# Optimization experiments

Measured on AMD Instinct MI355X. Metric: run time of the kernel, lower is better.

## Reference

```python
import jax, jax.numpy as jnp
import numpy as np

EPS = 1e-5        # torch LayerNorm default eps
INNER = 4
AFFECT_W = 0.3
BATCH = 65536
DIM = 128


def _ln(x, g, b):
    m = jnp.mean(x, axis=-1, keepdims=True)
    v = jnp.var(x, axis=-1, keepdims=True)
    return (x - m) * jax.lax.rsqrt(v + EPS) * g + b


def _gelu(x):
    return jax.nn.gelu(x, approximate=False)  # torch nn.GELU default (erf)


def setup_inputs() -> dict:
    key = jax.random.key(0)
    ks = jax.random.split(key, 18)
    B, d = BATCH, DIM

    def W(k, i, o):
        return jax.random.normal(k, (i, o), jnp.float32) / np.float32(np.sqrt(i))

    return {
        "x": jax.random.normal(ks[0], (B, d), jnp.float32),
        "y_init": jax.random.normal(ks[1], (B, d), jnp.float32),
        "affect_vec": jax.random.normal(ks[2], (B, 3), jnp.float32),
        "ln_latent_g": jnp.ones((3 * d,), jnp.float32), "ln_latent_b": jnp.zeros((3 * d,), jnp.float32),
        "ln_answer_g": jnp.ones((2 * d,), jnp.float32), "ln_answer_b": jnp.zeros((2 * d,), jnp.float32),
        "ln_z_g": jnp.ones((d,), jnp.float32), "ln_z_b": jnp.zeros((d,), jnp.float32),
        "lat_w1": W(ks[3], 3 * d, 2 * d), "lat_b1": jnp.zeros((2 * d,), jnp.float32),
        "lat_w2": W(ks[4], 2 * d, d), "lat_b2": jnp.zeros((d,), jnp.float32),
        "ans_w1": W(ks[5], 2 * d, 2 * d), "ans_b1": jnp.zeros((2 * d,), jnp.float32),
        "ans_w2": W(ks[6], 2 * d, d), "ans_b2": jnp.zeros((d,), jnp.float32),
        "aff_w": W(ks[7], 3, d), "aff_b": jnp.zeros((d,), jnp.float32),
        "gate_w": W(ks[8], 2 * d, 1), "gate_b": jnp.zeros((1,), jnp.float32),
        "q_w": W(ks[9], d, d), "q_b": jnp.zeros((d,), jnp.float32),
        "k_w": W(ks[10], d, d), "k_b": jnp.zeros((d,), jnp.float32),
        "v_w": W(ks[11], d, d), "v_b": jnp.zeros((d,), jnp.float32),
        "o_w": W(ks[12], d, d), "o_b": jnp.zeros((d,), jnp.float32),
        "pad_w1": W(ks[13], d, d // 2), "pad_b1": jnp.zeros((d // 2,), jnp.float32),
        "pad_w2": W(ks[14], d // 2, 3), "pad_b2": jnp.zeros((3,), jnp.float32),
        "K": 5,
    }


def _forward(x, y_init, affect_vec, ln_latent_g, ln_latent_b, ln_answer_g, ln_answer_b,
             ln_z_g, ln_z_b, lat_w1, lat_b1, lat_w2, lat_b2, ans_w1, ans_b1, ans_w2, ans_b2,
             aff_w, aff_b, gate_w, gate_b, q_w, q_b, k_w, k_b, v_w, v_b, o_w, o_b,
             pad_w1, pad_b1, pad_w2, pad_b2, K):
    d = x.shape[-1]
    scale = jnp.float32(d) ** -0.5
    y = y_init
    z = jnp.zeros_like(y)
    confs = []     # scalar gate means (detached, like .item() in torch)
    history = []   # list of [B, 1, d] z snapshots
    memory = []    # SoulKernel memory buffer: list of [d] rinse_state[0] snapshots
    for _ in range(K):
        for _ in range(INNER):
            li = _ln(jnp.concatenate([x, y, z], axis=-1), ln_latent_g, ln_latent_b)
            z_delta = _gelu(li @ lat_w1 + lat_b1) @ lat_w2 + lat_b2
            z = _ln(z + 0.3 * z_delta, ln_z_g, ln_z_b)
        affect_latent = jnp.tanh(affect_vec @ aff_w + aff_b)          # [B, d]
        gate = jax.nn.sigmoid(jnp.concatenate([z, affect_latent], axis=-1) @ gate_w + gate_b)  # [B, 1]
        z = z + AFFECT_W * gate * affect_latent
        confs.append(jax.lax.stop_gradient(jnp.mean(gate)))
        history.append(z[:, None, :])
        if len(history) > 1:
            seq = jnp.concatenate(history, axis=1)  # [B, t, d]
            Q = seq @ q_w + q_b
            Kt = seq @ k_w + k_b
            V = seq @ v_w + v_b
            attn = jax.nn.softmax(jnp.einsum('bsd,btd->bst', Q, Kt) * scale, axis=-1)
            attn_out = jnp.einsum('bst,btd->bsd', attn, V) @ o_w + o_b
            z = _ln(z + attn_out[:, -1, :], ln_z_g, ln_z_b)
        rinse = jnp.tanh(z + y)
        # SoulKernel (hope is computed but unused in the original)
        faith = jnp.sqrt(sum(confs) / len(confs))
        z = z + faith * 0.05 * z
        future = jnp.mean(jnp.stack(memory[-3:]), axis=0) if memory else jnp.zeros((d,), x.dtype)  # [d]
        bond = jnp.tanh(jax.lax.stop_gradient(jnp.mean(x * z)) + jax.lax.stop_gradient(jnp.mean(y * rinse)))
        z = z + 0.2 * bond * (future - z)
        rinse = jnp.tanh(rinse + future * 0.3)
        memory.append(jax.lax.stop_gradient(rinse[0]))
        ai = _ln(jnp.concatenate([y, z], axis=-1), ln_answer_g, ln_answer_b)
        y = y + 0.4 * (_gelu(ai @ ans_w1 + ans_b1) @ ans_w2 + ans_b2)
    pad = jnp.tanh(_gelu(z @ pad_w1 + pad_b1) @ pad_w2 + pad_b2)
    return y, jnp.stack(confs), pad


def reference(x, y_init, affect_vec, ln_latent_g, ln_latent_b, ln_answer_g, ln_answer_b,
              ln_z_g, ln_z_b, lat_w1, lat_b1, lat_w2, lat_b2, ans_w1, ans_b1, ans_w2, ans_b2,
              aff_w, aff_b, gate_w, gate_b, q_w, q_b, k_w, k_b, v_w, v_b, o_w, o_b,
              pad_w1, pad_b1, pad_w2, pad_b2, K):
    return _forward(x, y_init, affect_vec, ln_latent_g, ln_latent_b, ln_answer_g, ln_answer_b,
                    ln_z_g, ln_z_b, lat_w1, lat_b1, lat_w2, lat_b2, ans_w1, ans_b1, ans_w2, ans_b2,
                    aff_w, aff_b, gate_w, gate_b, q_w, q_b, k_w, k_b, v_w, v_b, o_w, o_b,
                    pad_w1, pad_b1, pad_w2, pad_b2, K)
```

## Files before the change

### kernel.cpp

```cpp
#include <hip/hip_runtime.h>
#include <math.h>


#define BATCH 65536
#define D 128
#define NSTEP 5
#define ROWS 32
#define NTHR 256
#define NBLK (BATCH / ROWS)
#define LN_EPS 1e-5f
#define ATT_SCALE 0.08838834764831845f
#define LDA 132
#define LDB 260

#define WS_Z    ((size_t)0)
#define WS_ZH   ((size_t)BATCH * D)
#define WS_PART (WS_ZH + (size_t)NSTEP * BATCH * D)
#define WS_SCAL (WS_PART + (size_t)NBLK * 4)
#define SC_FS   0
#define SC_B02  1
#define SC_CSUM 2
#define SC_FUT  16
#define SC_MEM  256
#define SC_R10  960

struct Args {
  const float *x, *y_init, *affect;
  const float *g_lat, *b_lat, *g_ans, *b_ans, *g_z, *b_z;
  const float *lw1, *lb1, *lw2, *lb2;
  const float *aw1, *ab1, *aw2, *ab2;
  const float *affw, *affb, *gw, *gb;
  const float *qw, *qb, *kw, *kb, *vw, *vb, *ow, *ob;
  const float *pw1, *pb1, *pw2, *pb2;
  float *Y, *conf, *pad;
  float *Z, *ZH, *PART, *SCAL;
};

__device__ __forceinline__ float4 ld4(const float* p) { return *(const float4*)p; }
__device__ __forceinline__ void st4(float* p, float4 v) { *(float4*)p = v; }
__device__ __forceinline__ float geluf(float v) { return 0.5f*v*(1.0f + erff(v*0.70710678118654752f)); }
__device__ __forceinline__ float dot4(float4 a, float4 b){ return a.x*b.x + a.y*b.y + a.z*b.z + a.w*b.w; }
__device__ __forceinline__ void accSQ(float4 v, float& S, float& Q) {
  S += v.x+v.y+v.z+v.w;
  Q += v.x*v.x + v.y*v.y + v.z*v.z + v.w*v.w;
}

template<int KDIM, int NPT>
__device__ __forceinline__ void mm_block(const float* __restrict__ W, int N,
                                         const float* As, int lda,
                                         int rg, int cg, float (&acc)[4][NPT])
{
  const float* a0 = As + (rg*4+0)*lda;
  const float* a1 = As + (rg*4+1)*lda;
  const float* a2 = As + (rg*4+2)*lda;
  const float* a3 = As + (rg*4+3)*lda;
  const float* wp = W + cg*NPT;
  #pragma unroll 4
  for (int k = 0; k < KDIM; ++k) {
    float w[NPT];
    if constexpr (NPT == 8) {
      float4 w0 = ld4(wp + (size_t)k*N);
      float4 w1 = ld4(wp + (size_t)k*N + 4);
      w[0]=w0.x; w[1]=w0.y; w[2]=w0.z; w[3]=w0.w;
      w[4]=w1.x; w[5]=w1.y; w[6]=w1.z; w[7]=w1.w;
    } else if constexpr (NPT == 4) {
      float4 w0 = ld4(wp + (size_t)k*N);
      w[0]=w0.x; w[1]=w0.y; w[2]=w0.z; w[3]=w0.w;
    } else {
      float2 w0 = *(const float2*)(wp + (size_t)k*N);
      w[0]=w0.x; w[1]=w0.y;
    }
    float av0=a0[k], av1=a1[k], av2=a2[k], av3=a3[k];
    #pragma unroll
    for (int c = 0; c < NPT; ++c) {
      acc[0][c] += av0*w[c];
      acc[1][c] += av1*w[c];
      acc[2][c] += av2*w[c];
      acc[3][c] += av3*w[c];
    }
  }
}

__device__ __forceinline__ void z_ln_update(const Args& A, int row0, int rg, int cg,
                                            const float (&add)[4][4])
{
  float4 g4 = ld4(A.g_z + cg*4);
  float4 b4 = ld4(A.b_z + cg*4);
  #pragma unroll
  for (int rr = 0; rr < 4; ++rr) {
    size_t off = (size_t)(row0 + rg*4 + rr)*D + cg*4;
    float4 z = ld4(A.Z + off);
    float v0 = z.x + add[rr][0];
    float v1 = z.y + add[rr][1];
    float v2 = z.z + add[rr][2];
    float v3 = z.w + add[rr][3];
    float S = v0+v1+v2+v3;
    float Q = v0*v0+v1*v1+v2*v2+v3*v3;
    S += __shfl_xor(S,1);  Q += __shfl_xor(Q,1);
    S += __shfl_xor(S,2);  Q += __shfl_xor(Q,2);
    S += __shfl_xor(S,4);  Q += __shfl_xor(Q,4);
    S += __shfl_xor(S,8);  Q += __shfl_xor(Q,8);
    S += __shfl_xor(S,16); Q += __shfl_xor(Q,16);
    float m  = S*(1.f/128.f);
    float rs = rsqrtf(Q*(1.f/128.f) - m*m + LN_EPS);
    float4 o;
    o.x = (v0-m)*rs*g4.x + b4.x;
    o.y = (v1-m)*rs*g4.y + b4.y;
    o.z = (v2-m)*rs*g4.z + b4.z;
    o.w = (v3-m)*rs*g4.w + b4.w;
    st4(A.Z + off, o);
  }
}

__device__ __forceinline__ void stage_raw(float* sA, const float* src, int row0, int t)
{
  for (int e4 = t; e4 < ROWS*32; e4 += NTHR) {
    int r = e4 >> 5, c4 = e4 & 31;
    st4(sA + r*LDA + c4*4, ld4(src + (size_t)(row0+r)*D + c4*4));
  }
}

__device__ __forceinline__ void epilogue_phase(const Args& A, float* sB, float* sM, float* sR,
                                               int row0, int t, int rg, int cg, int r8, int sub)
{
  const float fs  = A.SCAL[SC_FS];
  const float b02 = A.SCAL[SC_B02];
  const float a   = fs*(1.0f - b02);
  for (int e4 = t; e4 < ROWS*32; e4 += NTHR) {
    int r = e4 >> 5, c4 = e4 & 31;
    size_t off = (size_t)(row0 + r)*D + c4*4;
    float4 z = ld4(A.Z + off);
    float4 f = ld4(A.SCAL + SC_FUT + c4*4);
    z.x = z.x*a + b02*f.x;
    z.y = z.y*a + b02*f.y;
    z.z = z.z*a + b02*f.z;
    z.w = z.w*a + b02*f.w;
    st4(A.Z + off, z);
  }
  __syncthreads();
  {
    const float* yr = A.Y + (size_t)(row0 + r8)*D;
    const float* zr = A.Z + (size_t)(row0 + r8)*D;
    float S = 0.f, Q = 0.f;
    #pragma unroll
    for (int j = 0; j < 4; ++j) {
      int c = (sub + 8*j)*4;
      accSQ(ld4(yr + c), S, Q);
      accSQ(ld4(zr + c), S, Q);
    }
    S += __shfl_xor(S,1); Q += __shfl_xor(Q,1);
    S += __shfl_xor(S,2); Q += __shfl_xor(Q,2);
    S += __shfl_xor(S,4); Q += __shfl_xor(Q,4);
    if (sub == 0) {
      float m = S*(1.f/256.f);
      sM[r8] = m;
      sR[r8] = rsqrtf(Q*(1.f/256.f) - m*m + LN_EPS);
    }
  }
  __syncthreads();
  for (int e4 = t; e4 < ROWS*64; e4 += NTHR) {
    int r = e4 >> 6, c4 = e4 & 63;
    int k = c4*4;
    float m = sM[r], rs = sR[r];
    float4 v = (k < D) ? ld4(A.Y + (size_t)(row0+r)*D + k)
                       : ld4(A.Z + (size_t)(row0+r)*D + (k - D));
    float4 g = ld4(A.g_ans + k);
    float4 b = ld4(A.b_ans + k);
    float4 o;
    o.x = (v.x-m)*rs*g.x + b.x;
    o.y = (v.y-m)*rs*g.y + b.y;
    o.z = (v.z-m)*rs*g.z + b.z;
    o.w = (v.w-m)*rs*g.w + b.w;
    st4(sB + r*LDB + k, o);
  }
  __syncthreads();
  float acc[4][8] = {};
  mm_block<256,8>(A.aw1, 256, sB, LDB, rg, cg, acc);
  float4 b1a = ld4(A.ab1 + cg*8);
  float4 b1b = ld4(A.ab1 + cg*8 + 4);
  float h[4][8];
  #pragma unroll
  for (int rr = 0; rr < 4; ++rr) {
    h[rr][0]=geluf(acc[rr][0]+b1a.x); h[rr][1]=geluf(acc[rr][1]+b1a.y);
    h[rr][2]=geluf(acc[rr][2]+b1a.z); h[rr][3]=geluf(acc[rr][3]+b1a.w);
    h[rr][4]=geluf(acc[rr][4]+b1b.x); h[rr][5]=geluf(acc[rr][5]+b1b.y);
    h[rr][6]=geluf(acc[rr][6]+b1b.z); h[rr][7]=geluf(acc[rr][7]+b1b.w);
  }
  __syncthreads();
  #pragma unroll
  for (int rr = 0; rr < 4; ++rr) {
    float4 h0; h0.x=h[rr][0]; h0.y=h[rr][1]; h0.z=h[rr][2]; h0.w=h[rr][3];
    float4 h1; h1.x=h[rr][4]; h1.y=h[rr][5]; h1.z=h[rr][6]; h1.w=h[rr][7];
    st4(sB + (rg*4+rr)*LDB + cg*8,     h0);
    st4(sB + (rg*4+rr)*LDB + cg*8 + 4, h1);
  }
  __syncthreads();
  float acc2[4][4] = {};
  mm_block<256,4>(A.aw2, 128, sB, LDB, rg, cg, acc2);
  float4 b2 = ld4(A.ab2 + cg*4);
  #pragma unroll
  for (int rr = 0; rr < 4; ++rr) {
    size_t off = (size_t)(row0 + rg*4 + rr)*D + cg*4;
    float4 y = ld4(A.Y + off);
    y.x += 0.4f*(acc2[rr][0] + b2.x);
    y.y += 0.4f*(acc2[rr][1] + b2.y);
    y.z += 0.4f*(acc2[rr][2] + b2.z);
    y.w += 0.4f*(acc2[rr][3] + b2.w);
    st4(A.Y + off, y);
  }
  __syncthreads();
}

__global__ void prepK(Args A)
{
  size_t i  = (size_t)blockIdx.x*blockDim.x + threadIdx.x;
  size_t n4 = (size_t)BATCH*D/4;
  float4 zero; zero.x=0.f; zero.y=0.f; zero.z=0.f; zero.w=0.f;
  for (; i < n4; i += (size_t)gridDim.x*blockDim.x) {
    ((float4*)A.Z)[i] = zero;
    ((float4*)A.Y)[i] = ((const float4*)A.y_init)[i];
  }
}

template<int STEP>
__global__ __launch_bounds__(NTHR, 2) void stepK(Args A)
{
  __shared__ __align__(16) float sA[ROWS*LDA];
  __shared__ __align__(16) float sB[ROWS*LDB];
  __shared__ float sM[ROWS], sR[ROWS], sG[ROWS];
  __shared__ float sS[ROWS][8];
  __shared__ float sRed[4][2];

  const int t = threadIdx.x;
  const int row0 = blockIdx.x * ROWS;
  const int rg = t >> 5, cg = t & 31;
  const int r8 = t >> 3, sub = t & 7;

  if (STEP > 0)
    epilogue_phase(A, sB, sM, sR, row0, t, rg, cg, r8, sub);

  #pragma unroll 1
  for (int it = 0; it < 4; ++it) {
    {
      const float* xr = A.x + (size_t)(row0 + r8)*D;
      const float* yr = A.Y + (size_t)(row0 + r8)*D;
      const float* zr = A.Z + (size_t)(row0 + r8)*D;
      float S = 0.f, Q = 0.f;
      #pragma unroll
      for (int j = 0; j < 4; ++j) {
        int c = (sub + 8*j)*4;
        accSQ(ld4(xr + c), S, Q);
        accSQ(ld4(yr + c), S, Q);
        accSQ(ld4(zr + c), S, Q);
      }
      S += __shfl_xor(S,1); Q += __shfl_xor(Q,1);
      S += __shfl_xor(S,2); Q += __shfl_xor(Q,2);
      S += __shfl_xor(S,4); Q += __shfl_xor(Q,4);
      if (sub == 0) {
        float m = S*(1.f/384.f);
        sM[r8] = m;
        sR[r8] = rsqrtf(Q*(1.f/384.f) - m*m + LN_EPS);
      }
    }
    __syncthreads();
    float acc[4][8] = {};
    #pragma unroll 1
    for (int seg = 0; seg < 3; ++seg) {
      const float* src = (seg == 0) ? A.x : (seg == 1 ? (const float*)A.Y : (const float*)A.Z);
      for (int e4 = t; e4 < ROWS*32; e4 += NTHR) {
        int r = e4 >> 5, c4 = e4 & 31;
        float4 v = ld4(src + (size_t)(row0+r)*D + c4*4);
        float m = sM[r], rs = sR[r];
        int k = seg*D + c4*4;
        float4 g = ld4(A.g_lat + k);
        float4 b = ld4(A.b_lat + k);
        float4 o;
        o.x = (v.x-m)*rs*g.x + b.x;
        o.y = (v.y-m)*rs*g.y + b.y;
        o.z = (v.z-m)*rs*g.z + b.z;
        o.w = (v.w-m)*rs*g.w + b.w;
        st4(sA + r*LDA + c4*4, o);
      }
      __syncthreads();
      mm_block<128,8>(A.lw1 + (size_t)seg*D*256, 256, sA, LDA, rg, cg, acc);
      __syncthreads();
    }
    float4 l1a = ld4(A.lb1 + cg*8);
    float4 l1b = ld4(A.lb1 + cg*8 + 4);
    #pragma unroll
    for (int rr = 0; rr < 4; ++rr) {
      float4 h0, h1;
      h0.x = geluf(acc[rr][0]+l1a.x); h0.y = geluf(acc[rr][1]+l1a.y);
      h0.z = geluf(acc[rr][2]+l1a.z); h0.w = geluf(acc[rr][3]+l1a.w);
      h1.x = geluf(acc[rr][4]+l1b.x); h1.y = geluf(acc[rr][5]+l1b.y);
      h1.z = geluf(acc[rr][6]+l1b.z); h1.w = geluf(acc[rr][7]+l1b.w);
      st4(sB + (rg*4+rr)*LDB + cg*8,     h0);
      st4(sB + (rg*4+rr)*LDB + cg*8 + 4, h1);
    }
    __syncthreads();
    float acc2[4][4] = {};
    mm_block<256,4>(A.lw2, 128, sB, LDB, rg, cg, acc2);
    float4 l2 = ld4(A.lb2 + cg*4);
    float add[4][4];
    #pragma unroll
    for (int rr = 0; rr < 4; ++rr) {
      add[rr][0] = 0.3f*(acc2[rr][0]+l2.x);
      add[rr][1] = 0.3f*(acc2[rr][1]+l2.y);
      add[rr][2] = 0.3f*(acc2[rr][2]+l2.z);
      add[rr][3] = 0.3f*(acc2[rr][3]+l2.w);
    }
    z_ln_update(A, row0, rg, cg, add);
    __syncthreads();
  }

  {
    size_t row = (size_t)row0 + r8;
    const float* zr = A.Z + row*D;
    float af0 = A.affect[row*3+0];
    float af1 = A.affect[row*3+1];
    float af2 = A.affect[row*3+2];
    float dg = 0.f;
    #pragma unroll
    for (int j = 0; j < 4; ++j) {
      int c = (sub + 8*j)*4;
      float4 zv = ld4(zr + c);
      float4 g1 = ld4(A.gw + c);
      float4 g2 = ld4(A.gw + D + c);
      float4 w0 = ld4(A.affw + c);
      float4 w1 = ld4(A.affw + D + c);
      float4 w2 = ld4(A.affw + 2*D + c);
      float4 ab = ld4(A.affb + c);
      float4 al;
      al.x = tanhf(af0*w0.x + af1*w1.x + af2*w2.x + ab.x);
      al.y = tanhf(af0*w0.y + af1*w1.y + af2*w2.y + ab.y);
      al.z = tanhf(af0*w0.z + af1*w1.z + af2*w2.z + ab.z);
      al.w = tanhf(af0*w0.w + af1*w1.w + af2*w2.w + ab.w);
      st4(sA + r8*LDA + c, al);
      dg += dot4(zv, g1) + dot4(al, g2);
    }
    dg += __shfl_xor(dg,1);
    dg += __shfl_xor(dg,2);
    dg += __shfl_xor(dg,4);
    if (sub == 0) sG[r8] = 1.f/(1.f + expf(-(dg + A.gb[0])));
  }
  __syncthreads();
  {
    float* zhw = A.ZH + (size_t)STEP*BATCH*D;
    for (int e4 = t; e4 < ROWS*32; e4 += NTHR) {
      int r = e4 >> 5, c4 = e4 & 31;
      size_t off = (size_t)(row0+r)*D + c4*4;
      float4 z  = ld4(A.Z + off);
      float4 al = ld4(sA + r*LDA + c4*4);
      float g = 0.3f * sG[r];
      z.x += g*al.x; z.y += g*al.y; z.z += g*al.z; z.w += g*al.w;
      st4(A.Z + off, z);
      st4(zhw + off, z);
    }
  }
  __syncthreads();

  if (STEP > 0) {
    stage_raw(sA, A.Z, row0, t);
    __syncthreads();
    float qacc[4][4] = {};
    mm_block<128,4>(A.qw, 128, sA, LDA, rg, cg, qacc);
    float4 qb4 = ld4(A.qb + cg*4);
    #pragma unroll
    for (int rr = 0; rr < 4; ++rr) {
      float4 q;
      q.x=qacc[rr][0]+qb4.x; q.y=qacc[rr][1]+qb4.y;
      q.z=qacc[rr][2]+qb4.z; q.w=qacc[rr][3]+qb4.w;
      st4(sB + (rg*4+rr)*LDB + cg*4, q);
    }
    __syncthreads();
    #pragma unroll 1
    for (int j = 0; j <= STEP; ++j) {
      stage_raw(sA, A.ZH + (size_t)j*BATCH*D, row0, t);
      __syncthreads();
      float kacc[4][4] = {};
      mm_block<128,4>(A.kw, 128, sA, LDA, rg, cg, kacc);
      float4 kb4 = ld4(A.kb + cg*4);
      #pragma unroll
      for (int rr = 0; rr < 4; ++rr) {
        const float* qrow = sB + (rg*4+rr)*LDB + cg*4;
        float s = qrow[0]*(kacc[rr][0]+kb4.x) + qrow[1]*(kacc[rr][1]+kb4.y)
                + qrow[2]*(kacc[rr][2]+kb4.z) + qrow[3]*(kacc[rr][3]+kb4.w);
        s += __shfl_xor(s,1); s += __shfl_xor(s,2); s += __shfl_xor(s,4);
        s += __shfl_xor(s,8); s += __shfl_xor(s,16);
        if (cg == 0) sS[rg*4+rr][j] = s;
      }
      __syncthreads();
    }
    if (t < ROWS) {
      float mx = -3.0e38f;
      for (int j = 0; j <= STEP; ++j) { float v = sS[t][j]*ATT_SCALE; sS[t][j] = v; mx = fmaxf(mx, v); }
      float sum = 0.f;
      for (int j = 0; j <= STEP; ++j) { float p = expf(sS[t][j]-mx); sS[t][j] = p; sum += p; }
      float inv = 1.f/sum;
      for (int j = 0; j <= STEP; ++j) sS[t][j] *= inv;
    }
    __syncthreads();
    float ao[4][4] = {};
    #pragma unroll 1
    for (int j = 0; j <= STEP; ++j) {
      stage_raw(sA, A.ZH + (size_t)j*BATCH*D, row0, t);
      __syncthreads();
      float vacc[4][4] = {};
      mm_block<128,4>(A.vw, 128, sA, LDA, rg, cg, vacc);
      float4 vb4 = ld4(A.vb + cg*4);
      #pragma unroll
      for (int rr = 0; rr < 4; ++rr) {
        float p = sS[rg*4+rr][j];
        ao[rr][0] += p*(vacc[rr][0]+vb4.x);
        ao[rr][1] += p*(vacc[rr][1]+vb4.y);
        ao[rr][2] += p*(vacc[rr][2]+vb4.z);
        ao[rr][3] += p*(vacc[rr][3]+vb4.w);
      }
      __syncthreads();
    }
    #pragma unroll
    for (int rr = 0; rr < 4; ++rr) {
      float4 v; v.x=ao[rr][0]; v.y=ao[rr][1]; v.z=ao[rr][2]; v.w=ao[rr][3];
      st4(sA + (rg*4+rr)*LDA + cg*4, v);
    }
    __syncthreads();
    float oacc[4][4] = {};
    mm_block<128,4>(A.ow, 128, sA, LDA, rg, cg, oacc);
    float4 ob4 = ld4(A.ob + cg*4);
    float add[4][4];
    #pragma unroll
    for (int rr = 0; rr < 4; ++rr) {
      add[rr][0] = oacc[rr][0]+ob4.x;
      add[rr][1] = oacc[rr][1]+ob4.y;
      add[rr][2] = oacc[rr][2]+ob4.z;
      add[rr][3] = oacc[rr][3]+ob4.w;
    }
    z_ln_update(A, row0, rg, cg, add);
    __syncthreads();
  }

  {
    float sxz = 0.f, syr = 0.f;
    for (int e4 = t; e4 < ROWS*32; e4 += NTHR) {
      int r = e4 >> 5, c4 = e4 & 31;
      size_t off = (size_t)(row0+r)*D + c4*4;
      float4 xv = ld4(A.x + off);
      float4 zv = ld4(A.Z + off);
      float4 yv = ld4(A.Y + off);
      float4 rn;
      rn.x = tanhf(zv.x + yv.x);
      rn.y = tanhf(zv.y + yv.y);
      rn.z = tanhf(zv.z + yv.z);
      rn.w = tanhf(zv.w + yv.w);
      sxz += dot4(xv, zv);
      syr += dot4(yv, rn);
      if (blockIdx.x == 0 && r == 0)
        st4(A.SCAL + SC_R10 + c4*4, rn);
    }
    #pragma unroll
    for (int m2 = 1; m2 < 64; m2 <<= 1) { sxz += __shfl_xor(sxz,m2); syr += __shfl_xor(syr,m2); }
    if ((t & 63) == 0) { sRed[t>>6][0] = sxz; sRed[t>>6][1] = syr; }
    __syncthreads();
    if (t == 0) {
      float X = 0.f, Yv = 0.f, G = 0.f;
      #pragma unroll
      for (int w2 = 0; w2 < 4; ++w2) { X += sRed[w2][0]; Yv += sRed[w2][1]; }
      #pragma unroll
      for (int r = 0; r < ROWS; ++r) G += sG[r];
      float* p = A.PART + (size_t)blockIdx.x*4;
      p[0] = G; p[1] = X; p[2] = Yv;
    }
  }
}

template<int STEP>
__global__ void redK(Args A)
{
  __shared__ float sRed[4][3];
  const int t = threadIdx.x;
  float sg = 0.f, sxz = 0.f, syr = 0.f;
  for (int b = t; b < NBLK; b += 256) {
    const float* p = A.PART + (size_t)b*4;
    sg += p[0]; sxz += p[1]; syr += p[2];
  }
  #pragma unroll
  for (int m = 1; m < 64; m <<= 1) {
    sg  += __shfl_xor(sg,m);
    sxz += __shfl_xor(sxz,m);
    syr += __shfl_xor(syr,m);
  }
  if ((t & 63) == 0) { int w = t>>6; sRed[w][0]=sg; sRed[w][1]=sxz; sRed[w][2]=syr; }
  __syncthreads();
  if (t == 0) {
    float G=0.f, X=0.f, Yv=0.f;
    #pragma unroll
    for (int w = 0; w < 4; ++w) { G += sRed[w][0]; X += sRed[w][1]; Yv += sRed[w][2]; }
    float conf = G * (1.f/(float)BATCH);
    float csum = conf + (STEP == 0 ? 0.f : A.SCAL[SC_CSUM]);
    A.SCAL[SC_CSUM] = csum;
    A.conf[STEP] = conf;
    float faith = sqrtf(csum / (float)(STEP+1));
    float fs = 1.f + 0.05f*faith;
    float bond = tanhf((fs*X + Yv) * (1.f/((float)BATCH*(float)D)));
    A.SCAL[SC_FS]  = fs;
    A.SCAL[SC_B02] = 0.2f*bond;
  }
  if (t < D) {
    float fut = 0.f;
    if (STEP > 0) {
      int lo = (STEP-3 < 0) ? 0 : STEP-3;
      float s = 0.f;
      for (int j = lo; j < STEP; ++j) s += A.SCAL[SC_MEM + j*D + t];
      fut = s / (float)(STEP - lo);
    }
    A.SCAL[SC_FUT + t] = fut;
    A.SCAL[SC_MEM + STEP*D + t] = tanhf(A.SCAL[SC_R10 + t] + 0.3f*fut);
  }
}

__global__ __launch_bounds__(NTHR, 2) void finalK(Args A)
{
  __shared__ __align__(16) float sA[ROWS*LDA];
  __shared__ __align__(16) float sB[ROWS*LDB];
  __shared__ float sM[ROWS], sR[ROWS];
  const int t = threadIdx.x;
  const int row0 = blockIdx.x * ROWS;
  const int rg = t >> 5, cg = t & 31;
  const int r8 = t >> 3, sub = t & 7;

  epilogue_phase(A, sB, sM, sR, row0, t, rg, cg, r8, sub);

  stage_raw(sA, A.Z, row0, t);
  __syncthreads();
  float acc[4][2] = {};
  mm_block<128,2>(A.pw1, 64, sA, LDA, rg, cg, acc);
  float2 pb = *(const float2*)(A.pb1 + cg*2);
  #pragma unroll
  for (int rr = 0; rr < 4; ++rr) {
    sB[(rg*4+rr)*LDB + cg*2 + 0] = geluf(acc[rr][0] + pb.x);
    sB[(rg*4+rr)*LDB + cg*2 + 1] = geluf(acc[rr][1] + pb.y);
  }
  __syncthreads();
  {
    float o0=0.f, o1=0.f, o2=0.f;
    #pragma unroll
    for (int jj = 0; jj < 8; ++jj) {
      int j = sub*8 + jj;
      float p = sB[r8*LDB + j];
      o0 += p*A.pw2[j*3+0];
      o1 += p*A.pw2[j*3+1];
      o2 += p*A.pw2[j*3+2];
    }
    o0 += __shfl_xor(o0,1); o0 += __shfl_xor(o0,2); o0 += __shfl_xor(o0,4);
    o1 += __shfl_xor(o1,1); o1 += __shfl_xor(o1,2); o1 += __shfl_xor(o1,4);
    o2 += __shfl_xor(o2,1); o2 += __shfl_xor(o2,2); o2 += __shfl_xor(o2,4);
    if (sub == 0) {
      size_t ro = (size_t)(row0 + r8)*3;
      A.pad[ro+0] = tanhf(o0 + A.pb2[0]);
      A.pad[ro+1] = tanhf(o1 + A.pb2[1]);
      A.pad[ro+2] = tanhf(o2 + A.pb2[2]);
    }
  }
}

extern "C" void kernel_launch(void* const* d_in, const int* in_sizes, int n_in,
                              void* d_out, int out_size, void* d_ws, size_t ws_size,
                              hipStream_t stream)
{
  (void)in_sizes; (void)n_in; (void)out_size; (void)ws_size;
  Args a;
  a.x      = (const float*)d_in[0];
  a.y_init = (const float*)d_in[1];
  a.affect = (const float*)d_in[2];
  a.g_lat  = (const float*)d_in[3];
  a.b_lat  = (const float*)d_in[4];
  a.g_ans  = (const float*)d_in[5];
  a.b_ans  = (const float*)d_in[6];
  a.g_z    = (const float*)d_in[7];
  a.b_z    = (const float*)d_in[8];
  a.lw1    = (const float*)d_in[9];
  a.lb1    = (const float*)d_in[10];
  a.lw2    = (const float*)d_in[11];
  a.lb2    = (const float*)d_in[12];
  a.aw1    = (const float*)d_in[13];
  a.ab1    = (const float*)d_in[14];
  a.aw2    = (const float*)d_in[15];
  a.ab2    = (const float*)d_in[16];
  a.affw   = (const float*)d_in[17];
  a.affb   = (const float*)d_in[18];
  a.gw     = (const float*)d_in[19];
  a.gb     = (const float*)d_in[20];
  a.qw     = (const float*)d_in[21];
  a.qb     = (const float*)d_in[22];
  a.kw     = (const float*)d_in[23];
  a.kb     = (const float*)d_in[24];
  a.vw     = (const float*)d_in[25];
  a.vb     = (const float*)d_in[26];
  a.ow     = (const float*)d_in[27];
  a.ob     = (const float*)d_in[28];
  a.pw1    = (const float*)d_in[29];
  a.pb1    = (const float*)d_in[30];
  a.pw2    = (const float*)d_in[31];
  a.pb2    = (const float*)d_in[32];
  float* out = (float*)d_out;
  a.Y    = out;
  a.conf = out + (size_t)BATCH*D;
  a.pad  = a.conf + NSTEP;
  float* ws = (float*)d_ws;
  a.Z    = ws + WS_Z;
  a.ZH   = ws + WS_ZH;
  a.PART = ws + WS_PART;
  a.SCAL = ws + WS_SCAL;

  prepK<<<dim3(2048), dim3(256), 0, stream>>>(a);
  stepK<0><<<dim3(NBLK), dim3(NTHR), 0, stream>>>(a);
  redK<0><<<dim3(1), dim3(256), 0, stream>>>(a);
  stepK<1><<<dim3(NBLK), dim3(NTHR), 0, stream>>>(a);
  redK<1><<<dim3(1), dim3(256), 0, stream>>>(a);
  stepK<2><<<dim3(NBLK), dim3(NTHR), 0, stream>>>(a);
  redK<2><<<dim3(1), dim3(256), 0, stream>>>(a);
  stepK<3><<<dim3(NBLK), dim3(NTHR), 0, stream>>>(a);
  redK<3><<<dim3(1), dim3(256), 0, stream>>>(a);
  stepK<4><<<dim3(NBLK), dim3(NTHR), 0, stream>>>(a);
  redK<4><<<dim3(1), dim3(256), 0, stream>>>(a);
  finalK<<<dim3(NBLK), dim3(NTHR), 0, stream>>>(a);
}
```

Measured before the change: 8.326 ms.

## Merge shared buffers into one tile and raise occupancy to four blocks per CU

Collapses the two shared-memory tiles (sA, sB) into one unified buffer sU and raises launch bounds from 2 to 4 blocks per multiprocessor, which cuts LDS per block roughly in half. Query projections are kept in registers rather than shared memory, and barriers inside the attention loops move so the single buffer can be reused safely. Fixed-count staging loops are also unrolled. The tighter launch bound can force register spilling and adds barriers where the buffers used to be separate.

After: 10.24 ms. +23.0%, slower.

```diff
diff --git a/kernel.cpp b/kernel.cpp
--- a/kernel.cpp
+++ b/kernel.cpp
@@ -4,19 +4,20 @@
 
 #define BATCH 65536
 #define D 128
+#define BD ((size_t)BATCH * D)
 #define NSTEP 5
 #define ROWS 32
 #define NTHR 256
 #define NBLK (BATCH / ROWS)
 #define LN_EPS 1e-5f
 #define ATT_SCALE 0.08838834764831845f
-#define LDA 132
-#define LDB 260
+#define LDU 260
 
 #define WS_Z    ((size_t)0)
-#define WS_ZH   ((size_t)BATCH * D)
-#define WS_PART (WS_ZH + (size_t)NSTEP * BATCH * D)
-#define WS_SCAL (WS_PART + (size_t)NBLK * 4)
+#define WS_ZH   (BD)
+#define WS_PART (WS_ZH + 5*BD)
+#define WS_SCAL (WS_PART + (size_t)NBLK*4)
+
 #define SC_FS   0
 #define SC_B02  1
 #define SC_CSUM 2
@@ -112,21 +113,25 @@
   }
 }
 
-__device__ __forceinline__ void stage_raw(float* sA, const float* src, int row0, int t)
-{
-  for (int e4 = t; e4 < ROWS*32; e4 += NTHR) {
+__device__ __forceinline__ void stage_raw(float* sU, const float* src, int row0, int t)
+{
+  #pragma unroll
+  for (int p = 0; p < 4; ++p) {
+    int e4 = t + p*NTHR;
     int r = e4 >> 5, c4 = e4 & 31;
-    st4(sA + r*LDA + c4*4, ld4(src + (size_t)(row0+r)*D + c4*4));
-  }
-}
-
-__device__ __forceinline__ void epilogue_phase(const Args& A, float* sB, float* sM, float* sR,
+    st4(sU + r*LDU + c4*4, ld4(src + (size_t)(row0+r)*D + c4*4));
+  }
+}
+
+__device__ __forceinline__ void epilogue_phase(const Args& A, float* sU, float* sM, float* sR,
                                                int row0, int t, int rg, int cg, int r8, int sub)
 {
   const float fs  = A.SCAL[SC_FS];
   const float b02 = A.SCAL[SC_B02];
   const float a   = fs*(1.0f - b02);
-  for (int e4 = t; e4 < ROWS*32; e4 += NTHR) {
+  #pragma unroll
+  for (int p = 0; p < 4; ++p) {
+    int e4 = t + p*NTHR;
     int r = e4 >> 5, c4 = e4 & 31;
     size_t off = (size_t)(row0 + r)*D + c4*4;
     float4 z = ld4(A.Z + off);
@@ -171,11 +176,11 @@
     o.y = (v.y-m)*rs*g.y + b.y;
     o.z = (v.z-m)*rs*g.z + b.z;
     o.w = (v.w-m)*rs*g.w + b.w;
-    st4(sB + r*LDB + k, o);
+    st4(sU + r*LDU + k, o);
   }
   __syncthreads();
   float acc[4][8] = {};
-  mm_block<256,8>(A.aw1, 256, sB, LDB, rg, cg, acc);
+  mm_block<256,8>(A.aw1, 256, sU, LDU, rg, cg, acc);
   float4 b1a = ld4(A.ab1 + cg*8);
   float4 b1b = ld4(A.ab1 + cg*8 + 4);
   float h[4][8];
@@ -191,12 +196,12 @@
   for (int rr = 0; rr < 4; ++rr) {
     float4 h0; h0.x=h[rr][0]; h0.y=h[rr][1]; h0.z=h[rr][2]; h0.w=h[rr][3];
     float4 h1; h1.x=h[rr][4]; h1.y=h[rr][5]; h1.z=h[rr][6]; h1.w=h[rr][7];
-    st4(sB + (rg*4+rr)*LDB + cg*8,     h0);
-    st4(sB + (rg*4+rr)*LDB + cg*8 + 4, h1);
+    st4(sU + (rg*4+rr)*LDU + cg*8,     h0);
+    st4(sU + (rg*4+rr)*LDU + cg*8 + 4, h1);
   }
   __syncthreads();
   float acc2[4][4] = {};
-  mm_block<256,4>(A.aw2, 128, sB, LDB, rg, cg, acc2);
+  mm_block<256,4>(A.aw2, 128, sU, LDU, rg, cg, acc2);
   float4 b2 = ld4(A.ab2 + cg*4);
   #pragma unroll
   for (int rr = 0; rr < 4; ++rr) {
@@ -214,7 +219,7 @@
 __global__ void prepK(Args A)
 {
   size_t i  = (size_t)blockIdx.x*blockDim.x + threadIdx.x;
-  size_t n4 = (size_t)BATCH*D/4;
+  size_t n4 = BD/4;
   float4 zero; zero.x=0.f; zero.y=0.f; zero.z=0.f; zero.w=0.f;
   for (; i < n4; i += (size_t)gridDim.x*blockDim.x) {
     ((float4*)A.Z)[i] = zero;
@@ -223,10 +228,9 @@
 }
 
 template<int STEP>
-__global__ __launch_bounds__(NTHR, 2) void stepK(Args A)
-{
-  __shared__ __align__(16) float sA[ROWS*LDA];
-  __shared__ __align__(16) float sB[ROWS*LDB];
+__global__ __launch_bounds__(NTHR, 4) void stepK(Args A)
+{
+  __shared__ __align__(16) float sU[ROWS*LDU];
   __shared__ float sM[ROWS], sR[ROWS], sG[ROWS];
   __shared__ float sS[ROWS][8];
   __shared__ float sRed[4][2];
@@ -237,7 +241,7 @@
   const int r8 = t >> 3, sub = t & 7;
 
   if (STEP > 0)
-    epilogue_phase(A, sB, sM, sR, row0, t, rg, cg, r8, sub);
+    epilogue_phase(A, sU, sM, sR, row0, t, rg, cg, r8, sub);
 
   #pragma unroll 1
   for (int it = 0; it < 4; ++it) {
@@ -267,7 +271,9 @@
     #pragma unroll 1
     for (int seg = 0; seg < 3; ++seg) {
       const float* src = (seg == 0) ? A.x : (seg == 1 ? (const float*)A.Y : (const float*)A.Z);
-      for (int e4 = t; e4 < ROWS*32; e4 += NTHR) {
+      #pragma unroll
+      for (int p = 0; p < 4; ++p) {
+        int e4 = t + p*NTHR;
         int r = e4 >> 5, c4 = e4 & 31;
         float4 v = ld4(src + (size_t)(row0+r)*D + c4*4);
         float m = sM[r], rs = sR[r];
@@ -279,10 +285,10 @@
         o.y = (v.y-m)*rs*g.y + b.y;
         o.z = (v.z-m)*rs*g.z + b.z;
         o.w = (v.w-m)*rs*g.w + b.w;
-        st4(sA + r*LDA + c4*4, o);
+        st4(sU + r*LDU + c4*4, o);
       }
       __syncthreads();
-      mm_block<128,8>(A.lw1 + (size_t)seg*D*256, 256, sA, LDA, rg, cg, acc);
+      mm_block<128,8>(A.lw1 + (size_t)seg*D*256, 256, sU, LDU, rg, cg, acc);
       __syncthreads();
     }
     float4 l1a = ld4(A.lb1 + cg*8);
@@ -294,12 +300,12 @@
       h0.z = geluf(acc[rr][2]+l1a.z); h0.w = geluf(acc[rr][3]+l1a.w);
       h1.x = geluf(acc[rr][4]+l1b.x); h1.y = geluf(acc[rr][5]+l1b.y);
       h1.z = geluf(acc[rr][6]+l1b.z); h1.w = geluf(acc[rr][7]+l1b.w);
-      st4(sB + (rg*4+rr)*LDB + cg*8,     h0);
-      st4(sB + (rg*4+rr)*LDB + cg*8 + 4, h1);
+      st4(sU + (rg*4+rr)*LDU + cg*8,     h0);
+      st4(sU + (rg*4+rr)*LDU + cg*8 + 4, h1);
     }
     __syncthreads();
     float acc2[4][4] = {};
-    mm_block<256,4>(A.lw2, 128, sB, LDB, rg, cg, acc2);
+    mm_block<256,4>(A.lw2, 128, sU, LDU, rg, cg, acc2);
     float4 l2 = ld4(A.lb2 + cg*4);
     float add[4][4];
     #pragma unroll
@@ -335,7 +341,7 @@
       al.y = tanhf(af0*w0.y + af1*w1.y + af2*w2.y + ab.y);
       al.z = tanhf(af0*w0.z + af1*w1.z + af2*w2.z + ab.z);
       al.w = tanhf(af0*w0.w + af1*w1.w + af2*w2.w + ab.w);
-      st4(sA + r8*LDA + c, al);
+      st4(sU + r8*LDU + c, al);
       dg += dot4(zv, g1) + dot4(al, g2);
     }
     dg += __shfl_xor(dg,1);
@@ -345,12 +351,14 @@
   }
   __syncthreads();
   {
-    float* zhw = A.ZH + (size_t)STEP*BATCH*D;
-    for (int e4 = t; e4 < ROWS*32; e4 += NTHR) {
+    float* zhw = A.ZH + (size_t)STEP*BD;
+    #pragma unroll
+    for (int p = 0; p < 4; ++p) {
+      int e4 = t + p*NTHR;
       int r = e4 >> 5, c4 = e4 & 31;
       size_t off = (size_t)(row0+r)*D + c4*4;
       float4 z  = ld4(A.Z + off);
-      float4 al = ld4(sA + r*LDA + c4*4);
+      float4 al = ld4(sU + r*LDU + c4*4);
       float g = 0.3f * sG[r];
       z.x += g*al.x; z.y += g*al.y; z.z += g*al.z; z.w += g*al.w;
       st4(A.Z + off, z);
@@ -360,37 +368,37 @@
   __syncthreads();
 
   if (STEP > 0) {
-    stage_raw(sA, A.Z, row0, t);
-    __syncthreads();
-    float qacc[4][4] = {};
-    mm_block<128,4>(A.qw, 128, sA, LDA, rg, cg, qacc);
-    float4 qb4 = ld4(A.qb + cg*4);
-    #pragma unroll
-    for (int rr = 0; rr < 4; ++rr) {
-      float4 q;
-      q.x=qacc[rr][0]+qb4.x; q.y=qacc[rr][1]+qb4.y;
-      q.z=qacc[rr][2]+qb4.z; q.w=qacc[rr][3]+qb4.w;
-      st4(sB + (rg*4+rr)*LDB + cg*4, q);
-    }
-    __syncthreads();
+    stage_raw(sU, A.Z, row0, t);
+    __syncthreads();
+    float q[4][4];
+    {
+      float qacc[4][4] = {};
+      mm_block<128,4>(A.qw, 128, sU, LDU, rg, cg, qacc);
+      float4 qb4 = ld4(A.qb + cg*4);
+      #pragma unroll
+      for (int rr = 0; rr < 4; ++rr) {
+        q[rr][0]=qacc[rr][0]+qb4.x; q[rr][1]=qacc[rr][1]+qb4.y;
+        q[rr][2]=qacc[rr][2]+qb4.z; q[rr][3]=qacc[rr][3]+qb4.w;
+      }
+    }
     #pragma unroll 1
     for (int j = 0; j <= STEP; ++j) {
-      stage_raw(sA, A.ZH + (size_t)j*BATCH*D, row0, t);
+      __syncthreads();
+      stage_raw(sU, A.ZH + (size_t)j*BD, row0, t);
       __syncthreads();
       float kacc[4][4] = {};
-      mm_block<128,4>(A.kw, 128, sA, LDA, rg, cg, kacc);
+      mm_block<128,4>(A.kw, 128, sU, LDU, rg, cg, kacc);
       float4 kb4 = ld4(A.kb + cg*4);
       #pragma unroll
       for (int rr = 0; rr < 4; ++rr) {
-        const float* qrow = sB + (rg*4+rr)*LDB + cg*4;
-        float s = qrow[0]*(kacc[rr][0]+kb4.x) + qrow[1]*(kacc[rr][1]+kb4.y)
-                + qrow[2]*(kacc[rr][2]+kb4.z) + qrow[3]*(kacc[rr][3]+kb4.w);
+        float s = q[rr][0]*(kacc[rr][0]+kb4.x) + q[rr][1]*(kacc[rr][1]+kb4.y)
+                + q[rr][2]*(kacc[rr][2]+kb4.z) + q[rr][3]*(kacc[rr][3]+kb4.w);
         s += __shfl_xor(s,1); s += __shfl_xor(s,2); s += __shfl_xor(s,4);
         s += __shfl_xor(s,8); s += __shfl_xor(s,16);
         if (cg == 0) sS[rg*4+rr][j] = s;
       }
-      __syncthreads();
-    }
+    }
+    __syncthreads();
     if (t < ROWS) {
       float mx = -3.0e38f;
       for (int j = 0; j <= STEP; ++j) { float v = sS[t][j]*ATT_SCALE; sS[t][j] = v; mx = fmaxf(mx, v); }
@@ -403,10 +411,11 @@
     float ao[4][4] = {};
     #pragma unroll 1
     for (int j = 0; j <= STEP; ++j) {
-      stage_raw(sA, A.ZH + (size_t)j*BATCH*D, row0, t);
+      __syncthreads();
+      stage_raw(sU, A.ZH + (size_t)j*BD, row0, t);
       __syncthreads();
       float vacc[4][4] = {};
-      mm_block<128,4>(A.vw, 128, sA, LDA, rg, cg, vacc);
+      mm_block<128,4>(A.vw, 128, sU, LDU, rg, cg, vacc);
       float4 vb4 = ld4(A.vb + cg*4);
       #pragma unroll
       for (int rr = 0; rr < 4; ++rr) {
@@ -416,16 +425,16 @@
         ao[rr][2] += p*(vacc[rr][2]+vb4.z);
         ao[rr][3] += p*(vacc[rr][3]+vb4.w);
       }
-      __syncthreads();
-    }
+    }
+    __syncthreads();
     #pragma unroll
     for (int rr = 0; rr < 4; ++rr) {
       float4 v; v.x=ao[rr][0]; v.y=ao[rr][1]; v.z=ao[rr][2]; v.w=ao[rr][3];
-      st4(sA + (rg*4+rr)*LDA + cg*4, v);
+      st4(sU + (rg*4+rr)*LDU + cg*4, v);
     }
     __syncthreads();
     float oacc[4][4] = {};
-    mm_block<128,4>(A.ow, 128, sA, LDA, rg, cg, oacc);
+    mm_block<128,4>(A.ow, 128, sU, LDU, rg, cg, oacc);
     float4 ob4 = ld4(A.ob + cg*4);
     float add[4][4];
     #pragma unroll
@@ -441,7 +450,9 @@
 
   {
     float sxz = 0.f, syr = 0.f;
-    for (int e4 = t; e4 < ROWS*32; e4 += NTHR) {
+    #pragma unroll
+    for (int p = 0; p < 4; ++p) {
+      int e4 = t + p*NTHR;
       int r = e4 >> 5, c4 = e4 & 31;
       size_t off = (size_t)(row0+r)*D + c4*4;
       float4 xv = ld4(A.x + off);
@@ -518,27 +529,27 @@
   }
 }
 
-__global__ __launch_bounds__(NTHR, 2) void finalK(Args A)
-{
-  __shared__ __align__(16) float sA[ROWS*LDA];
-  __shared__ __align__(16) float sB[ROWS*LDB];
+__global__ __launch_bounds__(NTHR, 4) void finalK(Args A)
+{
+  __shared__ __align__(16) float sU[ROWS*LDU];
   __shared__ float sM[ROWS], sR[ROWS];
   const int t = threadIdx.x;
   const int row0 = blockIdx.x * ROWS;
   const int rg = t >> 5, cg = t & 31;
   const int r8 = t >> 3, sub = t & 7;
 
-  epilogue_phase(A, sB, sM, sR, row0, t, rg, cg, r8, sub);
-
-  stage_raw(sA, A.Z, row0, t);
+  epilogue_phase(A, sU, sM, sR, row0, t, rg, cg, r8, sub);
+
+  stage_raw(sU, A.Z, row0, t);
   __syncthreads();
   float acc[4][2] = {};
-  mm_block<128,2>(A.pw1, 64, sA, LDA, rg, cg, acc);
+  mm_block<128,2>(A.pw1, 64, sU, LDU, rg, cg, acc);
   float2 pb = *(const float2*)(A.pb1 + cg*2);
+  __syncthreads();
   #pragma unroll
   for (int rr = 0; rr < 4; ++rr) {
-    sB[(rg*4+rr)*LDB + cg*2 + 0] = geluf(acc[rr][0] + pb.x);
-    sB[(rg*4+rr)*LDB + cg*2 + 1] = geluf(acc[rr][1] + pb.y);
+    sU[(rg*4+rr)*LDU + 128 + cg*2 + 0] = geluf(acc[rr][0] + pb.x);
+    sU[(rg*4+rr)*LDU + 128 + cg*2 + 1] = geluf(acc[rr][1] + pb.y);
   }
   __syncthreads();
   {
@@ -546,7 +557,7 @@
     #pragma unroll
     for (int jj = 0; jj < 8; ++jj) {
       int j = sub*8 + jj;
-      float p = sB[r8*LDB + j];
+      float p = sU[r8*LDU + 128 + j];
       o0 += p*A.pw2[j*3+0];
       o1 += p*A.pw2[j*3+1];
       o2 += p*A.pw2[j*3+2];
@@ -604,7 +615,7 @@
   a.pb2    = (const float*)d_in[32];
   float* out = (float*)d_out;
   a.Y    = out;
-  a.conf = out + (size_t)BATCH*D;
+  a.conf = out + BD;
   a.pad  = a.conf + NSTEP;
   float* ws = (float*)d_ws;
   a.Z    = ws + WS_Z;
```

## Cache per-step K/V projections in workspace instead of recomputing history

Applied to the files above, without the earlier changes.

When the workspace is large enough, each step computes K and V projections of the new z once and stores them, so later steps read cached K/V rather than re-projecting every past z through k_w and v_w. This removes a quadratic number of small matmuls per block at the cost of extra workspace memory and global reads. The change also stages all three LayerNorm segments at once to cut barriers in the latent matmul, unrolls the staging loops, and raises the launch-bounds occupancy hint to 3 blocks per CU, which may force register spills. A fallback path keeps the recompute behaviour when the workspace is too small.

Result: slower. 11.36 ms (+36.4%).

```diff
diff --git a/kernel.cpp b/kernel.cpp
--- a/kernel.cpp
+++ b/kernel.cpp
@@ -4,6 +4,7 @@
 
 #define BATCH 65536
 #define D 128
+#define BD ((size_t)BATCH * D)
 #define NSTEP 5
 #define ROWS 32
 #define NTHR 256
@@ -14,9 +15,12 @@
 #define LDB 260
 
 #define WS_Z    ((size_t)0)
-#define WS_ZH   ((size_t)BATCH * D)
-#define WS_PART (WS_ZH + (size_t)NSTEP * BATCH * D)
-#define WS_SCAL (WS_PART + (size_t)NBLK * 4)
+#define WS_H1   (BD)
+#define WS_PART (WS_H1 + 5*BD)
+#define WS_SCAL (WS_PART + (size_t)NBLK*4)
+#define WS_H2   (WS_SCAL + 2048)
+#define WS_KV_END (WS_H2 + 5*BD)
+
 #define SC_FS   0
 #define SC_B02  1
 #define SC_CSUM 2
@@ -33,7 +37,8 @@
   const float *qw, *qb, *kw, *kb, *vw, *vb, *ow, *ob;
   const float *pw1, *pb1, *pw2, *pb2;
   float *Y, *conf, *pad;
-  float *Z, *ZH, *PART, *SCAL;
+  float *Z, *H1, *H2, *PART, *SCAL;
+  int useKV;
 };
 
 __device__ __forceinline__ float4 ld4(const float* p) { return *(const float4*)p; }
@@ -114,9 +119,51 @@
 
 __device__ __forceinline__ void stage_raw(float* sA, const float* src, int row0, int t)
 {
-  for (int e4 = t; e4 < ROWS*32; e4 += NTHR) {
+  #pragma unroll
+  for (int p = 0; p < 4; ++p) {
+    int e4 = t + p*NTHR;
     int r = e4 >> 5, c4 = e4 & 31;
     st4(sA + r*LDA + c4*4, ld4(src + (size_t)(row0+r)*D + c4*4));
+  }
+}
+
+__device__ __forceinline__ void stage_cat(const Args& A, float* sA, float* sB,
+                                          int row0, int t, const float* sM, const float* sR)
+{
+  #pragma unroll
+  for (int p = 0; p < 4; ++p) {
+    int e4 = t + p*NTHR;
+    int r = e4 >> 5, c4 = e4 & 31;
+    float m = sM[r], rs = sR[r];
+    size_t roff = (size_t)(row0+r)*D + c4*4;
+    int k0 = c4*4;
+    {
+      float4 v = ld4(A.x + roff);
+      float4 g = ld4(A.g_lat + k0);
+      float4 b = ld4(A.b_lat + k0);
+      float4 o;
+      o.x=(v.x-m)*rs*g.x+b.x; o.y=(v.y-m)*rs*g.y+b.y;
+      o.z=(v.z-m)*rs*g.z+b.z; o.w=(v.w-m)*rs*g.w+b.w;
+      st4(sA + r*LDA + k0, o);
+    }
+    {
+      float4 v = ld4(A.Y + roff);
+      float4 g = ld4(A.g_lat + D + k0);
+      float4 b = ld4(A.b_lat + D + k0);
+      float4 o;
+      o.x=(v.x-m)*rs*g.x+b.x; o.y=(v.y-m)*rs*g.y+b.y;
+      o.z=(v.z-m)*rs*g.z+b.z; o.w=(v.w-m)*rs*g.w+b.w;
+      st4(sB + r*LDB + k0, o);
+    }
+    {
+      float4 v = ld4(A.Z + roff);
+      float4 g = ld4(A.g_lat + 2*D + k0);
+      float4 b = ld4(A.b_lat + 2*D + k0);
+      float4 o;
+      o.x=(v.x-m)*rs*g.x+b.x; o.y=(v.y-m)*rs*g.y+b.y;
+      o.z=(v.z-m)*rs*g.z+b.z; o.w=(v.w-m)*rs*g.w+b.w;
+      st4(sB + r*LDB + 132 + k0, o);
+    }
   }
 }
 
@@ -126,7 +173,9 @@
   const float fs  = A.SCAL[SC_FS];
   const float b02 = A.SCAL[SC_B02];
   const float a   = fs*(1.0f - b02);
-  for (int e4 = t; e4 < ROWS*32; e4 += NTHR) {
+  #pragma unroll
+  for (int p = 0; p < 4; ++p) {
+    int e4 = t + p*NTHR;
     int r = e4 >> 5, c4 = e4 & 31;
     size_t off = (size_t)(row0 + r)*D + c4*4;
     float4 z = ld4(A.Z + off);
@@ -214,7 +263,7 @@
 __global__ void prepK(Args A)
 {
   size_t i  = (size_t)blockIdx.x*blockDim.x + threadIdx.x;
-  size_t n4 = (size_t)BATCH*D/4;
+  size_t n4 = BD/4;
   float4 zero; zero.x=0.f; zero.y=0.f; zero.z=0.f; zero.w=0.f;
   for (; i < n4; i += (size_t)gridDim.x*blockDim.x) {
     ((float4*)A.Z)[i] = zero;
@@ -223,7 +272,7 @@
 }
 
 template<int STEP>
-__global__ __launch_bounds__(NTHR, 2) void stepK(Args A)
+__global__ __launch_bounds__(NTHR, 3) void stepK(Args A)
 {
   __shared__ __align__(16) float sA[ROWS*LDA];
   __shared__ __align__(16) float sB[ROWS*LDB];
@@ -263,28 +312,13 @@
       }
     }
     __syncthreads();
+    stage_cat(A, sA, sB, row0, t, sM, sR);
+    __syncthreads();
     float acc[4][8] = {};
-    #pragma unroll 1
-    for (int seg = 0; seg < 3; ++seg) {
-      const float* src = (seg == 0) ? A.x : (seg == 1 ? (const float*)A.Y : (const float*)A.Z);
-      for (int e4 = t; e4 < ROWS*32; e4 += NTHR) {
-        int r = e4 >> 5, c4 = e4 & 31;
-        float4 v = ld4(src + (size_t)(row0+r)*D + c4*4);
-        float m = sM[r], rs = sR[r];
-        int k = seg*D + c4*4;
-        float4 g = ld4(A.g_lat + k);
-        float4 b = ld4(A.b_lat + k);
-        float4 o;
-        o.x = (v.x-m)*rs*g.x + b.x;
-        o.y = (v.y-m)*rs*g.y + b.y;
-        o.z = (v.z-m)*rs*g.z + b.z;
-        o.w = (v.w-m)*rs*g.w + b.w;
-        st4(sA + r*LDA + c4*4, o);
-      }
-      __syncthreads();
-      mm_block<128,8>(A.lw1 + (size_t)seg*D*256, 256, sA, LDA, rg, cg, acc);
-      __syncthreads();
-    }
+    mm_block<128,8>(A.lw1,                   256, sA,       LDA, rg, cg, acc);
+    mm_block<128,8>(A.lw1 + (size_t)D*256,   256, sB,       LDB, rg, cg, acc);
+    mm_block<128,8>(A.lw1 + (size_t)2*D*256, 256, sB + 132, LDB, rg, cg, acc);
+    __syncthreads();
     float4 l1a = ld4(A.lb1 + cg*8);
     float4 l1b = ld4(A.lb1 + cg*8 + 4);
     #pragma unroll
@@ -345,8 +379,10 @@
   }
   __syncthreads();
   {
-    float* zhw = A.ZH + (size_t)STEP*BATCH*D;
-    for (int e4 = t; e4 < ROWS*32; e4 += NTHR) {
+    float* zhw = A.H1 + (size_t)STEP*BD;
+    #pragma unroll
+    for (int p = 0; p < 4; ++p) {
+      int e4 = t + p*NTHR;
       int r = e4 >> 5, c4 = e4 & 31;
       size_t off = (size_t)(row0+r)*D + c4*4;
       float4 z  = ld4(A.Z + off);
@@ -354,43 +390,80 @@
       float g = 0.3f * sG[r];
       z.x += g*al.x; z.y += g*al.y; z.z += g*al.z; z.w += g*al.w;
       st4(A.Z + off, z);
-      st4(zhw + off, z);
-    }
-  }
-  __syncthreads();
-
+      if (!A.useKV) st4(zhw + off, z);
+    }
+  }
+  __syncthreads();
+
+  float q[4][4];
+  if (A.useKV || STEP > 0) {
+    stage_raw(sA, A.Z, row0, t);
+    __syncthreads();
+  }
+  if (A.useKV) {
+    float kacc[4][4] = {}, vacc[4][4] = {};
+    mm_block<128,4>(A.kw, 128, sA, LDA, rg, cg, kacc);
+    mm_block<128,4>(A.vw, 128, sA, LDA, rg, cg, vacc);
+    float4 kb4 = ld4(A.kb + cg*4);
+    float4 vb4 = ld4(A.vb + cg*4);
+    float* KH = A.H1 + (size_t)STEP*BD;
+    float* VH = A.H2 + (size_t)STEP*BD;
+    #pragma unroll
+    for (int rr = 0; rr < 4; ++rr) {
+      size_t off = (size_t)(row0 + rg*4 + rr)*D + cg*4;
+      float4 kv; kv.x=kacc[rr][0]+kb4.x; kv.y=kacc[rr][1]+kb4.y;
+                 kv.z=kacc[rr][2]+kb4.z; kv.w=kacc[rr][3]+kb4.w;
+      float4 vv; vv.x=vacc[rr][0]+vb4.x; vv.y=vacc[rr][1]+vb4.y;
+                 vv.z=vacc[rr][2]+vb4.z; vv.w=vacc[rr][3]+vb4.w;
+      st4(KH + off, kv);
+      st4(VH + off, vv);
+    }
+  }
   if (STEP > 0) {
-    stage_raw(sA, A.Z, row0, t);
-    __syncthreads();
     float qacc[4][4] = {};
     mm_block<128,4>(A.qw, 128, sA, LDA, rg, cg, qacc);
     float4 qb4 = ld4(A.qb + cg*4);
     #pragma unroll
     for (int rr = 0; rr < 4; ++rr) {
-      float4 q;
-      q.x=qacc[rr][0]+qb4.x; q.y=qacc[rr][1]+qb4.y;
-      q.z=qacc[rr][2]+qb4.z; q.w=qacc[rr][3]+qb4.w;
-      st4(sB + (rg*4+rr)*LDB + cg*4, q);
-    }
-    __syncthreads();
-    #pragma unroll 1
-    for (int j = 0; j <= STEP; ++j) {
-      stage_raw(sA, A.ZH + (size_t)j*BATCH*D, row0, t);
-      __syncthreads();
-      float kacc[4][4] = {};
-      mm_block<128,4>(A.kw, 128, sA, LDA, rg, cg, kacc);
-      float4 kb4 = ld4(A.kb + cg*4);
-      #pragma unroll
-      for (int rr = 0; rr < 4; ++rr) {
-        const float* qrow = sB + (rg*4+rr)*LDB + cg*4;
-        float s = qrow[0]*(kacc[rr][0]+kb4.x) + qrow[1]*(kacc[rr][1]+kb4.y)
-                + qrow[2]*(kacc[rr][2]+kb4.z) + qrow[3]*(kacc[rr][3]+kb4.w);
-        s += __shfl_xor(s,1); s += __shfl_xor(s,2); s += __shfl_xor(s,4);
-        s += __shfl_xor(s,8); s += __shfl_xor(s,16);
-        if (cg == 0) sS[rg*4+rr][j] = s;
+      q[rr][0]=qacc[rr][0]+qb4.x; q[rr][1]=qacc[rr][1]+qb4.y;
+      q[rr][2]=qacc[rr][2]+qb4.z; q[rr][3]=qacc[rr][3]+qb4.w;
+    }
+  }
+
+  if (STEP > 0) {
+    if (A.useKV) {
+      #pragma unroll 1
+      for (int j = 0; j <= STEP; ++j) {
+        const float* KH = A.H1 + (size_t)j*BD;
+        #pragma unroll
+        for (int rr = 0; rr < 4; ++rr) {
+          float4 kv = ld4(KH + (size_t)(row0 + rg*4 + rr)*D + cg*4);
+          float s = q[rr][0]*kv.x + q[rr][1]*kv.y + q[rr][2]*kv.z + q[rr][3]*kv.w;
+          s += __shfl_xor(s,1); s += __shfl_xor(s,2); s += __shfl_xor(s,4);
+          s += __shfl_xor(s,8); s += __shfl_xor(s,16);
+          if (cg == 0) sS[rg*4+rr][j] = s;
+        }
       }
-      __syncthreads();
-    }
+    } else {
+      #pragma unroll 1
+      for (int j = 0; j <= STEP; ++j) {
+        __syncthreads();
+        stage_raw(sA, A.H1 + (size_t)j*BD, row0, t);
+        __syncthreads();
+        float kacc[4][4] = {};
+        mm_block<128,4>(A.kw, 128, sA, LDA, rg, cg, kacc);
+        float4 kb4 = ld4(A.kb + cg*4);
+        #pragma unroll
+        for (int rr = 0; rr < 4; ++rr) {
+          float s = q[rr][0]*(kacc[rr][0]+kb4.x) + q[rr][1]*(kacc[rr][1]+kb4.y)
+                  + q[rr][2]*(kacc[rr][2]+kb4.z) + q[rr][3]*(kacc[rr][3]+kb4.w);
+          s += __shfl_xor(s,1); s += __shfl_xor(s,2); s += __shfl_xor(s,4);
+          s += __shfl_xor(s,8); s += __shfl_xor(s,16);
+          if (cg == 0) sS[rg*4+rr][j] = s;
+        }
+      }
+    }
+    __syncthreads();
     if (t < ROWS) {
       float mx = -3.0e38f;
       for (int j = 0; j <= STEP; ++j) { float v = sS[t][j]*ATT_SCALE; sS[t][j] = v; mx = fmaxf(mx, v); }
@@ -401,20 +474,35 @@
     }
     __syncthreads();
     float ao[4][4] = {};
-    #pragma unroll 1
-    for (int j = 0; j <= STEP; ++j) {
-      stage_raw(sA, A.ZH + (size_t)j*BATCH*D, row0, t);
-      __syncthreads();
-      float vacc[4][4] = {};
-      mm_block<128,4>(A.vw, 128, sA, LDA, rg, cg, vacc);
-      float4 vb4 = ld4(A.vb + cg*4);
-      #pragma unroll
-      for (int rr = 0; rr < 4; ++rr) {
-        float p = sS[rg*4+rr][j];
-        ao[rr][0] += p*(vacc[rr][0]+vb4.x);
-        ao[rr][1] += p*(vacc[rr][1]+vb4.y);
-        ao[rr][2] += p*(vacc[rr][2]+vb4.z);
-        ao[rr][3] += p*(vacc[rr][3]+vb4.w);
+    if (A.useKV) {
+      #pragma unroll 1
+      for (int j = 0; j <= STEP; ++j) {
+        const float* VH = A.H2 + (size_t)j*BD;
+        #pragma unroll
+        for (int rr = 0; rr < 4; ++rr) {
+          float p = sS[rg*4+rr][j];
+          float4 vv = ld4(VH + (size_t)(row0 + rg*4 + rr)*D + cg*4);
+          ao[rr][0] += p*vv.x; ao[rr][1] += p*vv.y;
+          ao[rr][2] += p*vv.z; ao[rr][3] += p*vv.w;
+        }
+      }
+    } else {
+      #pragma unroll 1
+      for (int j = 0; j <= STEP; ++j) {
+        __syncthreads();
+        stage_raw(sA, A.H1 + (size_t)j*BD, row0, t);
+        __syncthreads();
+        float vacc[4][4] = {};
+        mm_block<128,4>(A.vw, 128, sA, LDA, rg, cg, vacc);
+        float4 vb4 = ld4(A.vb + cg*4);
+        #pragma unroll
+        for (int rr = 0; rr < 4; ++rr) {
+          float p = sS[rg*4+rr][j];
+          ao[rr][0] += p*(vacc[rr][0]+vb4.x);
+          ao[rr][1] += p*(vacc[rr][1]+vb4.y);
+          ao[rr][2] += p*(vacc[rr][2]+vb4.z);
+          ao[rr][3] += p*(vacc[rr][3]+vb4.w);
+        }
       }
       __syncthreads();
     }
@@ -441,7 +529,9 @@
 
   {
     float sxz = 0.f, syr = 0.f;
-    for (int e4 = t; e4 < ROWS*32; e4 += NTHR) {
+    #pragma unroll
+    for (int p = 0; p < 4; ++p) {
+      int e4 = t + p*NTHR;
       int r = e4 >> 5, c4 = e4 & 31;
       size_t off = (size_t)(row0+r)*D + c4*4;
       float4 xv = ld4(A.x + off);
@@ -518,7 +608,7 @@
   }
 }
 
-__global__ __launch_bounds__(NTHR, 2) void finalK(Args A)
+__global__ __launch_bounds__(NTHR, 3) void finalK(Args A)
 {
   __shared__ __align__(16) float sA[ROWS*LDA];
   __shared__ __align__(16) float sB[ROWS*LDB];
@@ -535,6 +625,7 @@
   float acc[4][2] = {};
   mm_block<128,2>(A.pw1, 64, sA, LDA, rg, cg, acc);
   float2 pb = *(const float2*)(A.pb1 + cg*2);
+  __syncthreads();
   #pragma unroll
   for (int rr = 0; rr < 4; ++rr) {
     sB[(rg*4+rr)*LDB + cg*2 + 0] = geluf(acc[rr][0] + pb.x);
@@ -567,7 +658,7 @@
                               void* d_out, int out_size, void* d_ws, size_t ws_size,
                               hipStream_t stream)
 {
-  (void)in_sizes; (void)n_in; (void)out_size; (void)ws_size;
+  (void)in_sizes; (void)n_in; (void)out_size;
   Args a;
   a.x      = (const float*)d_in[0];
   a.y_init = (const float*)d_in[1];
@@ -604,13 +695,15 @@
   a.pb2    = (const float*)d_in[32];
   float* out = (float*)d_out;
   a.Y    = out;
-  a.conf = out + (size_t)BATCH*D;
+  a.conf = out + BD;
   a.pad  = a.conf + NSTEP;
   float* ws = (float*)d_ws;
   a.Z    = ws + WS_Z;
-  a.ZH   = ws + WS_ZH;
+  a.H1   = ws + WS_H1;
   a.PART = ws + WS_PART;
   a.SCAL = ws + WS_SCAL;
+  a.H2   = ws + WS_H2;
+  a.useKV = (ws_size >= WS_KV_END * sizeof(float)) ? 1 : 0;
 
   prepK<<<dim3(2048), dim3(256), 0, stream>>>(a);
   stepK<0><<<dim3(NBLK), dim3(NTHR), 0, stream>>>(a);
```
